# Kernel optimization log

Measured on AMD Instinct MI355X. Metric: run time of the kernel, lower is better.

## Reference

```python
import jax, jax.numpy as jnp
import numpy as np

ANG_RES = 5
USE_MASK = True
EPS = 1e-12  # torch F.normalize eps


def setup_inputs() -> dict:
    key = jax.random.key(0)
    kq, kk, kv = jax.random.split(key, 3)
    shape = (4, 64, 25, 64, 64)  # (b, c, n=angRes^2, h, w)
    return {
        "token_q": jax.random.normal(kq, shape, dtype=jnp.float32),
        "token_k": jax.random.normal(kk, shape, dtype=jnp.float32),
        "token_v": jax.random.normal(kv, shape, dtype=jnp.float32),
    }


def _unfold(x, u):
    # 'b c (u v) h w -> b (h u) (c v w)'
    b, c, n, h, w = x.shape
    v = n // u
    x = x.reshape(b, c, u, v, h, w)
    x = x.transpose(0, 4, 2, 1, 3, 5)  # (b, h, u, c, v, w)
    return x.reshape(b, h * u, c * v * w)


def _fold(x, u, c, h, w):
    # 'b (h u) (c v w) -> b c (u v) h w'
    b = x.shape[0]
    v = u
    x = x.reshape(b, h, u, c, v, w)
    x = x.transpose(0, 3, 2, 4, 1, 5)  # (b, c, u, v, h, w)
    return x.reshape(b, c, u * v, h, w)


def _l2norm(x, axis):
    n = jnp.sqrt(jnp.sum(x * x, axis=axis, keepdims=True))
    return x / jnp.maximum(n, EPS)


def reference(token_q, token_k, token_v):
    b, c, n, h, w = token_q.shape
    u = ANG_RES
    q = _l2norm(_unfold(token_q, u), axis=-1)   # (b, S, D), S=h*u, D=c*u*w
    k = _l2norm(_unfold(token_k, u), axis=-1)   # normalize along feature dim (dim=-2 of k^T)
    vv = _unfold(token_v, u)
    att = jnp.einsum('bsd,btd->bst', q, k)      # cosine similarity scores (b, S, S)
    if USE_MASK:
        S = att.shape[-1]
        causal = jnp.tril(jnp.ones((S, S), dtype=bool))
        att = jnp.where(causal, att, jnp.float32(-1e15))
    att = jax.nn.softmax(att, axis=-1)
    out = jnp.einsum('bst,btd->bsd', att, vv)
    return _fold(out, u, c, h, w) + token_v
```

## Files before the change

### kernel.cpp

```cpp
#include <hip/hip_runtime.h>


#define STR_B 6553600
#define STR_C 102400
#define STR_N 4096
#define STR_H 64

typedef __bf16 bf16x8 __attribute__((ext_vector_type(8)));
typedef float f32x4 __attribute__((ext_vector_type(4)));
typedef unsigned int u32x4 __attribute__((ext_vector_type(4)));

__device__ __forceinline__ int taddr(int b, int s, int d) {
    int h = s / 5, u = s % 5;
    int c = d / 320;
    int r = d % 320;
    int v = r >> 6;
    int w = r & 63;
    return b * STR_B + c * STR_C + (u * 5 + v) * STR_N + h * STR_H + w;
}

__device__ __forceinline__ unsigned short f2bf(float f) {
    unsigned int u = __float_as_uint(f);
    u += 0x7fffu + ((u >> 16) & 1u);
    return (unsigned short)(u >> 16);
}

__device__ __forceinline__ u32x4 pack8(float4 v0, float4 v1) {
    u32x4 w;
    w.x = (unsigned)f2bf(v0.x) | ((unsigned)f2bf(v0.y) << 16);
    w.y = (unsigned)f2bf(v0.z) | ((unsigned)f2bf(v0.w) << 16);
    w.z = (unsigned)f2bf(v1.x) | ((unsigned)f2bf(v1.y) << 16);
    w.w = (unsigned)f2bf(v1.z) | ((unsigned)f2bf(v1.w) << 16);
    return w;
}

__device__ __forceinline__ void gload_lds16(const void* g, void* l) {
    __builtin_amdgcn_global_load_lds(
        (const __attribute__((address_space(1))) unsigned int*)g,
        (__attribute__((address_space(3))) unsigned int*)l,
        16, 0, 0);
}


__global__ __launch_bounds__(1024) void qk_prep_kernel(
        const float* __restrict__ q, const float* __restrict__ k,
        unsigned short* __restrict__ qb, unsigned short* __restrict__ kb,
        float* __restrict__ qinv, float* __restrict__ kinv) {
    int row = blockIdx.x;
    const float* src = (row < 1280) ? q : k;
    unsigned short* dst = (row < 1280) ? qb : kb;
    float* dinv = (row < 1280) ? qinv : kinv;
    int rr = (row < 1280) ? row : row - 1280;
    int b = rr / 320, s = rr % 320;
    int tid = threadIdx.x;
    unsigned short* drow = dst + (size_t)rr * 20480;
    float ss = 0.f;
#pragma unroll
    for (int p = 0; p < 5; ++p) {
        int d = (p * 1024 + tid) * 4;
        f32x4 v = __builtin_nontemporal_load((const f32x4*)(src + taddr(b, s, d)));
        ushort4 w;
        w.x = f2bf(v.x);
        w.y = f2bf(v.y);
        w.z = f2bf(v.z);
        w.w = f2bf(v.w);
        *(ushort4*)(drow + d) = w;
        ss += v.x * v.x + v.y * v.y + v.z * v.z + v.w * v.w;
    }
#pragma unroll
    for (int off = 32; off > 0; off >>= 1) ss += __shfl_xor(ss, off, 64);
    __shared__ float part[16];
    if ((tid & 63) == 0) part[tid >> 6] = ss;
    __syncthreads();
    if (tid == 0) {
        float tot = 0.f;
#pragma unroll
        for (int i = 0; i < 16; ++i) tot += part[i];
        dinv[rr] = 1.f / fmaxf(sqrtf(tot), 1e-12f);
    }
}

#define SPLIT 20
#define KC (20480 / SPLIT)

__global__ __launch_bounds__(256) void scores2_kernel(
        const unsigned short* __restrict__ qb, const unsigned short* __restrict__ kb,
        const float* __restrict__ qinv, const float* __restrict__ kinv,
        float* __restrict__ att) {
    __shared__ unsigned short lds_a[64 * 32];
    __shared__ unsigned short lds_b[64 * 32];
    int b = blockIdx.y;
    int tileid = blockIdx.x / SPLIT;
    int chunk = blockIdx.x % SPLIT;
    int si = 0, rem = tileid;
    while (rem > si) { rem -= (si + 1); ++si; }
    int ti = rem;
    int s0 = si * 64, t0 = ti * 64;

    int tid = threadIdx.x;
    int r = tid >> 2, cl = tid & 3;
    int cg = cl ^ ((r >> 1) & 3);
    const unsigned short* ga = qb + (size_t)(b * 320 + s0 + r) * 20480 + chunk * KC + cg * 8;
    const unsigned short* gk = kb + (size_t)(b * 320 + t0 + r) * 20480 + chunk * KC + cg * 8;
    unsigned short* la = &lds_a[tid * 8];
    unsigned short* lb = &lds_b[tid * 8];

    int lane = tid & 63, wid = tid >> 6;
    int wy = wid >> 1, wx = wid & 1;
    int quad = lane >> 4, l15 = lane & 15;

    f32x4 acc[2][2] = {};
    for (int kk = 0; kk < KC; kk += 32) {
        gload_lds16(ga, la);
        gload_lds16(gk, lb);
        ga += 32; gk += 32;
        __syncthreads();
        bf16x8 af[2], bf[2];
#pragma unroll
        for (int t = 0; t < 2; ++t) {
            int ra = wy * 32 + t * 16 + l15;
            int ca = quad ^ ((ra >> 1) & 3);
            af[t] = __builtin_bit_cast(bf16x8, *(const u32x4*)&lds_a[ra * 32 + ca * 8]);
            int rb = wx * 32 + t * 16 + l15;
            int cb = quad ^ ((rb >> 1) & 3);
            bf[t] = __builtin_bit_cast(bf16x8, *(const u32x4*)&lds_b[rb * 32 + cb * 8]);
        }
        __syncthreads();
#pragma unroll
        for (int tm = 0; tm < 2; ++tm)
#pragma unroll
            for (int tn = 0; tn < 2; ++tn)
                acc[tm][tn] = __builtin_amdgcn_mfma_f32_16x16x32_bf16(
                    af[tm], bf[tn], acc[tm][tn], 0, 0, 0);
    }
    float ki[2];
#pragma unroll
    for (int tn = 0; tn < 2; ++tn)
        ki[tn] = kinv[b * 320 + t0 + wx * 32 + tn * 16 + l15];
#pragma unroll
    for (int tm = 0; tm < 2; ++tm)
#pragma unroll
        for (int tn = 0; tn < 2; ++tn)
#pragma unroll
            for (int i = 0; i < 4; ++i) {
                int s = s0 + wy * 32 + tm * 16 + quad * 4 + i;
                int t = t0 + wx * 32 + tn * 16 + l15;
                if (t <= s)
                    atomicAdd(&att[(b * 320 + s) * 320 + t],
                              acc[tm][tn][i] * qinv[b * 320 + s] * ki[tn]);
            }
}

__global__ __launch_bounds__(256) void softmax_kernel(
        const float* __restrict__ att, unsigned short* __restrict__ p) {
    int row = blockIdx.x * 4 + (threadIdx.x >> 6);
    int lane = threadIdx.x & 63;
    int b = row / 320, s = row % 320;
    const float* ar = att + (b * 320 + s) * 320;
    float v[5];
    float m = -1e30f;
#pragma unroll
    for (int j = 0; j < 5; ++j) {
        int t = lane + j * 64;
        v[j] = (t <= s) ? ar[t] : -1e30f;
        m = fmaxf(m, v[j]);
    }
#pragma unroll
    for (int off = 32; off > 0; off >>= 1) m = fmaxf(m, __shfl_xor(m, off, 64));
    float sum = 0.f;
#pragma unroll
    for (int j = 0; j < 5; ++j) {
        int t = lane + j * 64;
        v[j] = (t <= s) ? __expf(v[j] - m) : 0.f;
        sum += v[j];
    }
#pragma unroll
    for (int off = 32; off > 0; off >>= 1) sum += __shfl_xor(sum, off, 64);
    float inv = 1.f / sum;
    unsigned short* pr = p + (b * 320 + s) * 320;
#pragma unroll
    for (int j = 0; j < 5; ++j) {
        int t = lane + j * 64;
        pr[t] = f2bf(v[j] * inv);
    }
}

__global__ __launch_bounds__(256) void v_prep_kernel(
        const float* __restrict__ vin, unsigned short* __restrict__ vT) {
    __shared__ unsigned short lt[64 * 68];
    int b = blockIdx.z;
    int t0 = blockIdx.y * 64;
    int d0 = blockIdx.x * 64;
    int tid = threadIdx.x;
    int tl0 = tid >> 4;
    int dl = (tid & 15) * 4;
#pragma unroll
    for (int p = 0; p < 4; ++p) {
        int tl = tl0 + p * 16;
        float4 v = *(const float4*)(vin + taddr(b, t0 + tl, d0 + dl));
        lt[(dl + 0) * 68 + tl] = f2bf(v.x);
        lt[(dl + 1) * 68 + tl] = f2bf(v.y);
        lt[(dl + 2) * 68 + tl] = f2bf(v.z);
        lt[(dl + 3) * 68 + tl] = f2bf(v.w);
    }
    __syncthreads();
    int tc = (tid & 15) * 4;
#pragma unroll
    for (int p = 0; p < 4; ++p) {
        int dr = tl0 + p * 16;
        ushort4 w;
        w.x = lt[dr * 68 + tc + 0];
        w.y = lt[dr * 68 + tc + 1];
        w.z = lt[dr * 68 + tc + 2];
        w.w = lt[dr * 68 + tc + 3];
        *(ushort4*)(vT + (size_t)(b * 20480 + d0 + dr) * 320 + t0 + tc) = w;
    }
}

__global__ __launch_bounds__(256) void pv2_kernel(
        const unsigned short* __restrict__ p, const unsigned short* __restrict__ vT,
        const float* __restrict__ vin, float* __restrict__ out) {
    __shared__ unsigned short lds_a[64 * 32];
    __shared__ unsigned short lds_b[64 * 32];
    int b = blockIdx.z;
    int s0 = blockIdx.y * 64;
    int d0 = blockIdx.x * 64;
    int tid = threadIdx.x;
    int r = tid >> 2, cl = tid & 3;
    int cg = cl ^ ((r >> 1) & 3);
    const unsigned short* ga = p + (size_t)(b * 320 + s0 + r) * 320 + cg * 8;
    const unsigned short* gv = vT + (size_t)(b * 20480 + d0 + r) * 320 + cg * 8;
    unsigned short* la = &lds_a[tid * 8];
    unsigned short* lb = &lds_b[tid * 8];

    int lane = tid & 63, wid = tid >> 6;
    int wy = wid >> 1, wx = wid & 1;
    int quad = lane >> 4, l15 = lane & 15;

    f32x4 acc[2][2] = {};
    int nk = (s0 + 64) >> 5;
    for (int kc = 0; kc < nk; ++kc) {
        gload_lds16(ga, la);
        gload_lds16(gv, lb);
        ga += 32; gv += 32;
        __syncthreads();
        bf16x8 af[2], bf[2];
#pragma unroll
        for (int t = 0; t < 2; ++t) {
            int ra = wy * 32 + t * 16 + l15;
            int ca = quad ^ ((ra >> 1) & 3);
            af[t] = __builtin_bit_cast(bf16x8, *(const u32x4*)&lds_a[ra * 32 + ca * 8]);
            int rb = wx * 32 + t * 16 + l15;
            int cb = quad ^ ((rb >> 1) & 3);
            bf[t] = __builtin_bit_cast(bf16x8, *(const u32x4*)&lds_b[rb * 32 + cb * 8]);
        }
        __syncthreads();
#pragma unroll
        for (int tm = 0; tm < 2; ++tm)
#pragma unroll
            for (int tn = 0; tn < 2; ++tn)
                acc[tm][tn] = __builtin_amdgcn_mfma_f32_16x16x32_bf16(
                    af[tm], bf[tn], acc[tm][tn], 0, 0, 0);
    }
#pragma unroll
    for (int tm = 0; tm < 2; ++tm)
#pragma unroll
        for (int tn = 0; tn < 2; ++tn)
#pragma unroll
            for (int i = 0; i < 4; ++i) {
                int s = s0 + wy * 32 + tm * 16 + quad * 4 + i;
                int d = d0 + wx * 32 + tn * 16 + l15;
                int a = taddr(b, s, d);
                out[a] = acc[tm][tn][i] + vin[a];
            }
}


__global__ __launch_bounds__(256) void norm_kernel(
        const float* __restrict__ q, const float* __restrict__ k,
        float* __restrict__ qinv, float* __restrict__ kinv) {
    int row = blockIdx.x;
    const float* src = (row < 1280) ? q : k;
    float* dst = (row < 1280) ? qinv : kinv;
    int rr = (row < 1280) ? row : row - 1280;
    int b = rr / 320, s = rr % 320;
    int tid = threadIdx.x;
    float ss = 0.f;
#pragma unroll
    for (int p = 0; p < 20; ++p) {
        int kk = (p * 256 + tid) * 4;
        const float4 v = *(const float4*)(src + taddr(b, s, kk));
        ss += v.x * v.x + v.y * v.y + v.z * v.z + v.w * v.w;
    }
#pragma unroll
    for (int off = 32; off > 0; off >>= 1) ss += __shfl_xor(ss, off, 64);
    __shared__ float part[4];
    if ((tid & 63) == 0) part[tid >> 6] = ss;
    __syncthreads();
    if (tid == 0) {
        float tot = part[0] + part[1] + part[2] + part[3];
        dst[rr] = 1.f / fmaxf(sqrtf(tot), 1e-12f);
    }
}

#define CHUNKS 10
#define KCHUNK 2048

__global__ __launch_bounds__(256) void scores_kernel(
        const float* __restrict__ q, const float* __restrict__ kmat,
        const float* __restrict__ qinv, const float* __restrict__ kinv,
        float* __restrict__ att) {
    __shared__ unsigned short lds_a[64 * 40];
    __shared__ unsigned short lds_b[64 * 40];
    int b = blockIdx.y;
    int tileid = blockIdx.x / CHUNKS;
    int chunk = blockIdx.x % CHUNKS;
    int si = 0, rem = tileid;
    while (rem > si) { rem -= (si + 1); ++si; }
    int ti = rem;
    int s0 = si * 64, t0 = ti * 64;
    int tid = threadIdx.x;
    int r = tid >> 2, koff = (tid & 3) * 8;
    int lane = tid & 63, wid = tid >> 6;
    int wy = wid >> 1, wx = wid & 1;
    int quad = lane >> 4, l15 = lane & 15;
    f32x4 acc[2][2] = {};
    for (int kk = 0; kk < KCHUNK; kk += 32) {
        int kg = chunk * KCHUNK + kk + koff;
        const float4* pa = (const float4*)(q + taddr(b, s0 + r, kg));
        *(u32x4*)&lds_a[r * 40 + koff] = pack8(pa[0], pa[1]);
        const float4* pb = (const float4*)(kmat + taddr(b, t0 + r, kg));
        *(u32x4*)&lds_b[r * 40 + koff] = pack8(pb[0], pb[1]);
        __syncthreads();
        bf16x8 af[2], bf[2];
#pragma unroll
        for (int t = 0; t < 2; ++t) {
            af[t] = __builtin_bit_cast(bf16x8,
                *(const u32x4*)&lds_a[(wy * 32 + t * 16 + l15) * 40 + quad * 8]);
            bf[t] = __builtin_bit_cast(bf16x8,
                *(const u32x4*)&lds_b[(wx * 32 + t * 16 + l15) * 40 + quad * 8]);
        }
#pragma unroll
        for (int tm = 0; tm < 2; ++tm)
#pragma unroll
            for (int tn = 0; tn < 2; ++tn)
                acc[tm][tn] = __builtin_amdgcn_mfma_f32_16x16x32_bf16(
                    af[tm], bf[tn], acc[tm][tn], 0, 0, 0);
        __syncthreads();
    }
#pragma unroll
    for (int tm = 0; tm < 2; ++tm)
#pragma unroll
        for (int tn = 0; tn < 2; ++tn)
#pragma unroll
            for (int i = 0; i < 4; ++i) {
                int s = s0 + wy * 32 + tm * 16 + quad * 4 + i;
                int t = t0 + wx * 32 + tn * 16 + l15;
                if (t <= s) {
                    float val = acc[tm][tn][i] * qinv[b * 320 + s] * kinv[b * 320 + t];
                    atomicAdd(&att[(b * 320 + s) * 320 + t], val);
                }
            }
}

__global__ __launch_bounds__(256) void pv_kernel(
        const unsigned short* __restrict__ p, const float* __restrict__ vin,
        float* __restrict__ out) {
    __shared__ unsigned short lds_a[64 * 40];
    __shared__ unsigned short lds_b[64 * 40];
    int b = blockIdx.z;
    int s0 = blockIdx.y * 64;
    int d0 = blockIdx.x * 64;
    int tid = threadIdx.x;
    int lane = tid & 63, wid = tid >> 6;
    int wy = wid >> 1, wx = wid & 1;
    int quad = lane >> 4, l15 = lane & 15;
    int ar = tid >> 2, akoff = (tid & 3) * 8;
    int bt = tid >> 4;
    int bd = (tid & 15) * 4;
    f32x4 acc[2][2] = {};
    int nk = (s0 + 64) >> 5;
    for (int kc = 0; kc < nk; ++kc) {
        int t0k = kc * 32;
        u32x4 aw = *(const u32x4*)(p + ((b * 320 + s0 + ar) * 320 + t0k + akoff));
        *(u32x4*)&lds_a[ar * 40 + akoff] = aw;
#pragma unroll
        for (int pp = 0; pp < 2; ++pp) {
            int tt = bt + pp * 16;
            float4 v = *(const float4*)(vin + taddr(b, t0k + tt, d0 + bd));
            lds_b[(bd + 0) * 40 + tt] = f2bf(v.x);
            lds_b[(bd + 1) * 40 + tt] = f2bf(v.y);
            lds_b[(bd + 2) * 40 + tt] = f2bf(v.z);
            lds_b[(bd + 3) * 40 + tt] = f2bf(v.w);
        }
        __syncthreads();
        bf16x8 af[2], bf[2];
#pragma unroll
        for (int t = 0; t < 2; ++t) {
            af[t] = __builtin_bit_cast(bf16x8,
                *(const u32x4*)&lds_a[(wy * 32 + t * 16 + l15) * 40 + quad * 8]);
            bf[t] = __builtin_bit_cast(bf16x8,
                *(const u32x4*)&lds_b[(wx * 32 + t * 16 + l15) * 40 + quad * 8]);
        }
#pragma unroll
        for (int tm = 0; tm < 2; ++tm)
#pragma unroll
            for (int tn = 0; tn < 2; ++tn)
                acc[tm][tn] = __builtin_amdgcn_mfma_f32_16x16x32_bf16(
                    af[tm], bf[tn], acc[tm][tn], 0, 0, 0);
        __syncthreads();
    }
#pragma unroll
    for (int tm = 0; tm < 2; ++tm)
#pragma unroll
        for (int tn = 0; tn < 2; ++tn)
#pragma unroll
            for (int i = 0; i < 4; ++i) {
                int s = s0 + wy * 32 + tm * 16 + quad * 4 + i;
                int d = d0 + wx * 32 + tn * 16 + l15;
                int a = taddr(b, s, d);
                out[a] = acc[tm][tn][i] + vin[a];
            }
}

extern "C" void kernel_launch(void* const* d_in, const int* in_sizes, int n_in,
                              void* d_out, int out_size, void* d_ws, size_t ws_size,
                              hipStream_t stream) {
    const float* q = (const float*)d_in[0];
    const float* k = (const float*)d_in[1];
    const float* v = (const float*)d_in[2];
    float* out = (float*)d_out;
    char* ws = (char*)d_ws;

    const size_t QB_BYTES = (size_t)4 * 320 * 20480 * 2;
    const size_t ATT_BYTES = (size_t)4 * 320 * 320 * 4;
    const size_t P_BYTES = (size_t)4 * 320 * 320 * 2;
    const size_t INV_BYTES = (size_t)4 * 320 * 4;
    const size_t NEED = 2 * QB_BYTES + ATT_BYTES + P_BYTES + 2 * INV_BYTES;

    if (ws_size >= NEED) {
        unsigned short* qb = (unsigned short*)ws;
        unsigned short* kb = (unsigned short*)(ws + QB_BYTES);
        float* att = (float*)(ws + 2 * QB_BYTES);
        unsigned short* p = (unsigned short*)(ws + 2 * QB_BYTES + ATT_BYTES);
        float* qinv = (float*)(ws + 2 * QB_BYTES + ATT_BYTES + P_BYTES);
        float* kinv = (float*)(ws + 2 * QB_BYTES + ATT_BYTES + P_BYTES + INV_BYTES);
        unsigned short* vT = (unsigned short*)ws;

        qk_prep_kernel<<<2560, 1024, 0, stream>>>(q, k, qb, kb, qinv, kinv);
        hipMemsetAsync(att, 0, ATT_BYTES, stream);
        scores2_kernel<<<dim3(15 * SPLIT, 4), 256, 0, stream>>>(qb, kb, qinv, kinv, att);
        softmax_kernel<<<320, 256, 0, stream>>>(att, p);
        v_prep_kernel<<<dim3(320, 5, 4), 256, 0, stream>>>(v, vT);
        pv2_kernel<<<dim3(320, 5, 4), 256, 0, stream>>>(p, vT, v, out);
    } else {
        float* qinv = (float*)ws;
        float* kinv = (float*)(ws + 5120);
        float* att = (float*)(ws + 10240);
        unsigned short* p = (unsigned short*)(ws + 10240 + ATT_BYTES);

        norm_kernel<<<2560, 256, 0, stream>>>(q, k, qinv, kinv);
        hipMemsetAsync(att, 0, ATT_BYTES, stream);
        scores_kernel<<<dim3(15 * CHUNKS, 4), 256, 0, stream>>>(q, k, qinv, kinv, att);
        softmax_kernel<<<320, 256, 0, stream>>>(att, p);
        pv_kernel<<<dim3(320, 5, 4), 256, 0, stream>>>(p, v, out);
    }
}
```

Before: 420.9 us.

## Double-buffer LDS in QK and PV GEMMs; fuse softmax with V transpose

The scores and PV kernels now use two LDS buffers per operand, issuing the global-to-LDS load for the next k-step before computing on the current one, so each k-step needs one barrier instead of two. The softmax and V-transpose kernels are merged into one launch whose first 320 blocks do softmax and the rest transpose V. This targets load latency exposed in the GEMM loops and one kernel launch gap. In exchange it doubles LDS per block, which may reduce occupancy. The merged kernel also makes softmax blocks reserve the transpose scratch LDS.

```diff
diff --git a/kernel.cpp b/kernel.cpp
--- a/kernel.cpp
+++ b/kernel.cpp
@@ -40,6 +40,26 @@
         (__attribute__((address_space(3))) unsigned int*)l,
         16, 0, 0);
 }
+
+#define QK_STEP(LA, LB)                                                          \
+    do {                                                                         \
+        bf16x8 af[2], bf[2];                                                     \
+        _Pragma("unroll")                                                        \
+        for (int t = 0; t < 2; ++t) {                                            \
+            int ra = wy * 32 + t * 16 + l15;                                     \
+            int ca = quad ^ ((ra >> 1) & 3);                                     \
+            af[t] = __builtin_bit_cast(bf16x8, *(const u32x4*)&LA[ra * 32 + ca * 8]); \
+            int rb = wx * 32 + t * 16 + l15;                                     \
+            int cb = quad ^ ((rb >> 1) & 3);                                     \
+            bf[t] = __builtin_bit_cast(bf16x8, *(const u32x4*)&LB[rb * 32 + cb * 8]); \
+        }                                                                        \
+        _Pragma("unroll")                                                        \
+        for (int tm = 0; tm < 2; ++tm)                                           \
+            _Pragma("unroll")                                                    \
+            for (int tn = 0; tn < 2; ++tn)                                       \
+                acc[tm][tn] = __builtin_amdgcn_mfma_f32_16x16x32_bf16(           \
+                    af[tm], bf[tn], acc[tm][tn], 0, 0, 0);                       \
+    } while (0)
 
 
 __global__ __launch_bounds__(1024) void qk_prep_kernel(
@@ -87,8 +107,10 @@
         const unsigned short* __restrict__ qb, const unsigned short* __restrict__ kb,
         const float* __restrict__ qinv, const float* __restrict__ kinv,
         float* __restrict__ att) {
-    __shared__ unsigned short lds_a[64 * 32];
-    __shared__ unsigned short lds_b[64 * 32];
+    __shared__ unsigned short lds_a0[64 * 32];
+    __shared__ unsigned short lds_a1[64 * 32];
+    __shared__ unsigned short lds_b0[64 * 32];
+    __shared__ unsigned short lds_b1[64 * 32];
     int b = blockIdx.y;
     int tileid = blockIdx.x / SPLIT;
     int chunk = blockIdx.x % SPLIT;
@@ -100,38 +122,32 @@
     int tid = threadIdx.x;
     int r = tid >> 2, cl = tid & 3;
     int cg = cl ^ ((r >> 1) & 3);
-    const unsigned short* ga = qb + (size_t)(b * 320 + s0 + r) * 20480 + chunk * KC + cg * 8;
-    const unsigned short* gk = kb + (size_t)(b * 320 + t0 + r) * 20480 + chunk * KC + cg * 8;
-    unsigned short* la = &lds_a[tid * 8];
-    unsigned short* lb = &lds_b[tid * 8];
+    const unsigned short* gab = qb + (size_t)(b * 320 + s0 + r) * 20480 + chunk * KC + cg * 8;
+    const unsigned short* gkb = kb + (size_t)(b * 320 + t0 + r) * 20480 + chunk * KC + cg * 8;
+    unsigned short* la0 = &lds_a0[tid * 8];
+    unsigned short* la1 = &lds_a1[tid * 8];
+    unsigned short* lb0 = &lds_b0[tid * 8];
+    unsigned short* lb1 = &lds_b1[tid * 8];
 
     int lane = tid & 63, wid = tid >> 6;
     int wy = wid >> 1, wx = wid & 1;
     int quad = lane >> 4, l15 = lane & 15;
 
     f32x4 acc[2][2] = {};
-    for (int kk = 0; kk < KC; kk += 32) {
-        gload_lds16(ga, la);
-        gload_lds16(gk, lb);
-        ga += 32; gk += 32;
-        __syncthreads();
-        bf16x8 af[2], bf[2];
-#pragma unroll
-        for (int t = 0; t < 2; ++t) {
-            int ra = wy * 32 + t * 16 + l15;
-            int ca = quad ^ ((ra >> 1) & 3);
-            af[t] = __builtin_bit_cast(bf16x8, *(const u32x4*)&lds_a[ra * 32 + ca * 8]);
-            int rb = wx * 32 + t * 16 + l15;
-            int cb = quad ^ ((rb >> 1) & 3);
-            bf[t] = __builtin_bit_cast(bf16x8, *(const u32x4*)&lds_b[rb * 32 + cb * 8]);
-        }
-        __syncthreads();
-#pragma unroll
-        for (int tm = 0; tm < 2; ++tm)
-#pragma unroll
-            for (int tn = 0; tn < 2; ++tn)
-                acc[tm][tn] = __builtin_amdgcn_mfma_f32_16x16x32_bf16(
-                    af[tm], bf[tn], acc[tm][tn], 0, 0, 0);
+    gload_lds16(gab, la0);
+    gload_lds16(gkb, lb0);
+    __syncthreads();
+    for (int kk = 0; kk < KC; kk += 64) {
+        gload_lds16(gab + kk + 32, la1);
+        gload_lds16(gkb + kk + 32, lb1);
+        QK_STEP(lds_a0, lds_b0);
+        __syncthreads();
+        if (kk + 64 < KC) {
+            gload_lds16(gab + kk + 64, la0);
+            gload_lds16(gkb + kk + 64, lb0);
+        }
+        QK_STEP(lds_a1, lds_b1);
+        __syncthreads();
     }
     float ki[2];
 #pragma unroll
@@ -149,6 +165,156 @@
                     atomicAdd(&att[(b * 320 + s) * 320 + t],
                               acc[tm][tn][i] * qinv[b * 320 + s] * ki[tn]);
             }
+}
+
+__global__ __launch_bounds__(256) void softmax_vprep_kernel(
+        const float* __restrict__ att, unsigned short* __restrict__ p,
+        const float* __restrict__ vin, unsigned short* __restrict__ vT) {
+    __shared__ unsigned short lt[64 * 68];
+    int bid = blockIdx.x;
+    int tid = threadIdx.x;
+    if (bid < 320) {
+        int row = bid * 4 + (tid >> 6);
+        int lane = tid & 63;
+        int b = row / 320, s = row % 320;
+        const float* ar = att + (b * 320 + s) * 320;
+        float v[5];
+        float m = -1e30f;
+#pragma unroll
+        for (int j = 0; j < 5; ++j) {
+            int t = lane + j * 64;
+            v[j] = (t <= s) ? ar[t] : -1e30f;
+            m = fmaxf(m, v[j]);
+        }
+#pragma unroll
+        for (int off = 32; off > 0; off >>= 1) m = fmaxf(m, __shfl_xor(m, off, 64));
+        float sum = 0.f;
+#pragma unroll
+        for (int j = 0; j < 5; ++j) {
+            int t = lane + j * 64;
+            v[j] = (t <= s) ? __expf(v[j] - m) : 0.f;
+            sum += v[j];
+        }
+#pragma unroll
+        for (int off = 32; off > 0; off >>= 1) sum += __shfl_xor(sum, off, 64);
+        float inv = 1.f / sum;
+        unsigned short* pr = p + (b * 320 + s) * 320;
+#pragma unroll
+        for (int j = 0; j < 5; ++j) {
+            int t = lane + j * 64;
+            pr[t] = f2bf(v[j] * inv);
+        }
+        return;
+    }
+    int idx = bid - 320;
+    int d0 = (idx % 320) * 64;
+    int t0 = ((idx / 320) % 5) * 64;
+    int b = idx / 1600;
+    int tl0 = tid >> 4;
+    int dl = (tid & 15) * 4;
+#pragma unroll
+    for (int pp = 0; pp < 4; ++pp) {
+        int tl = tl0 + pp * 16;
+        float4 v = *(const float4*)(vin + taddr(b, t0 + tl, d0 + dl));
+        lt[(dl + 0) * 68 + tl] = f2bf(v.x);
+        lt[(dl + 1) * 68 + tl] = f2bf(v.y);
+        lt[(dl + 2) * 68 + tl] = f2bf(v.z);
+        lt[(dl + 3) * 68 + tl] = f2bf(v.w);
+    }
+    __syncthreads();
+    int tc = (tid & 15) * 4;
+#pragma unroll
+    for (int pp = 0; pp < 4; ++pp) {
+        int dr = tl0 + pp * 16;
+        ushort4 w;
+        w.x = lt[dr * 68 + tc + 0];
+        w.y = lt[dr * 68 + tc + 1];
+        w.z = lt[dr * 68 + tc + 2];
+        w.w = lt[dr * 68 + tc + 3];
+        *(ushort4*)(vT + (size_t)(b * 20480 + d0 + dr) * 320 + t0 + tc) = w;
+    }
+}
+
+__global__ __launch_bounds__(256) void pv2_kernel(
+        const unsigned short* __restrict__ p, const unsigned short* __restrict__ vT,
+        const float* __restrict__ vin, float* __restrict__ out) {
+    __shared__ unsigned short lds_a0[64 * 32];
+    __shared__ unsigned short lds_a1[64 * 32];
+    __shared__ unsigned short lds_b0[64 * 32];
+    __shared__ unsigned short lds_b1[64 * 32];
+    int b = blockIdx.z;
+    int s0 = blockIdx.y * 64;
+    int d0 = blockIdx.x * 64;
+    int tid = threadIdx.x;
+    int r = tid >> 2, cl = tid & 3;
+    int cg = cl ^ ((r >> 1) & 3);
+    const unsigned short* gab = p + (size_t)(b * 320 + s0 + r) * 320 + cg * 8;
+    const unsigned short* gvb = vT + (size_t)(b * 20480 + d0 + r) * 320 + cg * 8;
+    unsigned short* la0 = &lds_a0[tid * 8];
+    unsigned short* la1 = &lds_a1[tid * 8];
+    unsigned short* lb0 = &lds_b0[tid * 8];
+    unsigned short* lb1 = &lds_b1[tid * 8];
+
+    int lane = tid & 63, wid = tid >> 6;
+    int wy = wid >> 1, wx = wid & 1;
+    int quad = lane >> 4, l15 = lane & 15;
+
+    f32x4 acc[2][2] = {};
+    int nk = (s0 + 64) >> 5;
+    gload_lds16(gab, la0);
+    gload_lds16(gvb, lb0);
+    __syncthreads();
+    for (int kc = 0; kc < nk; kc += 2) {
+        gload_lds16(gab + (kc + 1) * 32, la1);
+        gload_lds16(gvb + (kc + 1) * 32, lb1);
+        QK_STEP(lds_a0, lds_b0);
+        __syncthreads();
+        if (kc + 2 < nk) {
+            gload_lds16(gab + (kc + 2) * 32, la0);
+            gload_lds16(gvb + (kc + 2) * 32, lb0);
+        }
+        QK_STEP(lds_a1, lds_b1);
+        __syncthreads();
+    }
+#pragma unroll
+    for (int tm = 0; tm < 2; ++tm)
+#pragma unroll
+        for (int tn = 0; tn < 2; ++tn)
+#pragma unroll
+            for (int i = 0; i < 4; ++i) {
+                int s = s0 + wy * 32 + tm * 16 + quad * 4 + i;
+                int d = d0 + wx * 32 + tn * 16 + l15;
+                int a = taddr(b, s, d);
+                out[a] = acc[tm][tn][i] + vin[a];
+            }
+}
+
+
+__global__ __launch_bounds__(256) void norm_kernel(
+        const float* __restrict__ q, const float* __restrict__ k,
+        float* __restrict__ qinv, float* __restrict__ kinv) {
+    int row = blockIdx.x;
+    const float* src = (row < 1280) ? q : k;
+    float* dst = (row < 1280) ? qinv : kinv;
+    int rr = (row < 1280) ? row : row - 1280;
+    int b = rr / 320, s = rr % 320;
+    int tid = threadIdx.x;
+    float ss = 0.f;
+#pragma unroll
+    for (int p = 0; p < 20; ++p) {
+        int kk = (p * 256 + tid) * 4;
+        const float4 v = *(const float4*)(src + taddr(b, s, kk));
+        ss += v.x * v.x + v.y * v.y + v.z * v.z + v.w * v.w;
+    }
+#pragma unroll
+    for (int off = 32; off > 0; off >>= 1) ss += __shfl_xor(ss, off, 64);
+    __shared__ float part[4];
+    if ((tid & 63) == 0) part[tid >> 6] = ss;
+    __syncthreads();
+    if (tid == 0) {
+        float tot = part[0] + part[1] + part[2] + part[3];
+        dst[rr] = 1.f / fmaxf(sqrtf(tot), 1e-12f);
+    }
 }
 
 __global__ __launch_bounds__(256) void softmax_kernel(
@@ -182,124 +348,6 @@
     for (int j = 0; j < 5; ++j) {
         int t = lane + j * 64;
         pr[t] = f2bf(v[j] * inv);
-    }
-}
-
-__global__ __launch_bounds__(256) void v_prep_kernel(
-        const float* __restrict__ vin, unsigned short* __restrict__ vT) {
-    __shared__ unsigned short lt[64 * 68];
-    int b = blockIdx.z;
-    int t0 = blockIdx.y * 64;
-    int d0 = blockIdx.x * 64;
-    int tid = threadIdx.x;
-    int tl0 = tid >> 4;
-    int dl = (tid & 15) * 4;
-#pragma unroll
-    for (int p = 0; p < 4; ++p) {
-        int tl = tl0 + p * 16;
-        float4 v = *(const float4*)(vin + taddr(b, t0 + tl, d0 + dl));
-        lt[(dl + 0) * 68 + tl] = f2bf(v.x);
-        lt[(dl + 1) * 68 + tl] = f2bf(v.y);
-        lt[(dl + 2) * 68 + tl] = f2bf(v.z);
-        lt[(dl + 3) * 68 + tl] = f2bf(v.w);
-    }
-    __syncthreads();
-    int tc = (tid & 15) * 4;
-#pragma unroll
-    for (int p = 0; p < 4; ++p) {
-        int dr = tl0 + p * 16;
-        ushort4 w;
-        w.x = lt[dr * 68 + tc + 0];
-        w.y = lt[dr * 68 + tc + 1];
-        w.z = lt[dr * 68 + tc + 2];
-        w.w = lt[dr * 68 + tc + 3];
-        *(ushort4*)(vT + (size_t)(b * 20480 + d0 + dr) * 320 + t0 + tc) = w;
-    }
-}
-
-__global__ __launch_bounds__(256) void pv2_kernel(
-        const unsigned short* __restrict__ p, const unsigned short* __restrict__ vT,
-        const float* __restrict__ vin, float* __restrict__ out) {
-    __shared__ unsigned short lds_a[64 * 32];
-    __shared__ unsigned short lds_b[64 * 32];
-    int b = blockIdx.z;
-    int s0 = blockIdx.y * 64;
-    int d0 = blockIdx.x * 64;
-    int tid = threadIdx.x;
-    int r = tid >> 2, cl = tid & 3;
-    int cg = cl ^ ((r >> 1) & 3);
-    const unsigned short* ga = p + (size_t)(b * 320 + s0 + r) * 320 + cg * 8;
-    const unsigned short* gv = vT + (size_t)(b * 20480 + d0 + r) * 320 + cg * 8;
-    unsigned short* la = &lds_a[tid * 8];
-    unsigned short* lb = &lds_b[tid * 8];
-
-    int lane = tid & 63, wid = tid >> 6;
-    int wy = wid >> 1, wx = wid & 1;
-    int quad = lane >> 4, l15 = lane & 15;
-
-    f32x4 acc[2][2] = {};
-    int nk = (s0 + 64) >> 5;
-    for (int kc = 0; kc < nk; ++kc) {
-        gload_lds16(ga, la);
-        gload_lds16(gv, lb);
-        ga += 32; gv += 32;
-        __syncthreads();
-        bf16x8 af[2], bf[2];
-#pragma unroll
-        for (int t = 0; t < 2; ++t) {
-            int ra = wy * 32 + t * 16 + l15;
-            int ca = quad ^ ((ra >> 1) & 3);
-            af[t] = __builtin_bit_cast(bf16x8, *(const u32x4*)&lds_a[ra * 32 + ca * 8]);
-            int rb = wx * 32 + t * 16 + l15;
-            int cb = quad ^ ((rb >> 1) & 3);
-            bf[t] = __builtin_bit_cast(bf16x8, *(const u32x4*)&lds_b[rb * 32 + cb * 8]);
-        }
-        __syncthreads();
-#pragma unroll
-        for (int tm = 0; tm < 2; ++tm)
-#pragma unroll
-            for (int tn = 0; tn < 2; ++tn)
-                acc[tm][tn] = __builtin_amdgcn_mfma_f32_16x16x32_bf16(
-                    af[tm], bf[tn], acc[tm][tn], 0, 0, 0);
-    }
-#pragma unroll
-    for (int tm = 0; tm < 2; ++tm)
-#pragma unroll
-        for (int tn = 0; tn < 2; ++tn)
-#pragma unroll
-            for (int i = 0; i < 4; ++i) {
-                int s = s0 + wy * 32 + tm * 16 + quad * 4 + i;
-                int d = d0 + wx * 32 + tn * 16 + l15;
-                int a = taddr(b, s, d);
-                out[a] = acc[tm][tn][i] + vin[a];
-            }
-}
-
-
-__global__ __launch_bounds__(256) void norm_kernel(
-        const float* __restrict__ q, const float* __restrict__ k,
-        float* __restrict__ qinv, float* __restrict__ kinv) {
-    int row = blockIdx.x;
-    const float* src = (row < 1280) ? q : k;
-    float* dst = (row < 1280) ? qinv : kinv;
-    int rr = (row < 1280) ? row : row - 1280;
-    int b = rr / 320, s = rr % 320;
-    int tid = threadIdx.x;
-    float ss = 0.f;
-#pragma unroll
-    for (int p = 0; p < 20; ++p) {
-        int kk = (p * 256 + tid) * 4;
-        const float4 v = *(const float4*)(src + taddr(b, s, kk));
-        ss += v.x * v.x + v.y * v.y + v.z * v.z + v.w * v.w;
-    }
-#pragma unroll
-    for (int off = 32; off > 0; off >>= 1) ss += __shfl_xor(ss, off, 64);
-    __shared__ float part[4];
-    if ((tid & 63) == 0) part[tid >> 6] = ss;
-    __syncthreads();
-    if (tid == 0) {
-        float tot = part[0] + part[1] + part[2] + part[3];
-        dst[rr] = 1.f / fmaxf(sqrtf(tot), 1e-12f);
     }
 }
 
@@ -450,8 +498,7 @@
         qk_prep_kernel<<<2560, 1024, 0, stream>>>(q, k, qb, kb, qinv, kinv);
         hipMemsetAsync(att, 0, ATT_BYTES, stream);
         scores2_kernel<<<dim3(15 * SPLIT, 4), 256, 0, stream>>>(qb, kb, qinv, kinv, att);
-        softmax_kernel<<<320, 256, 0, stream>>>(att, p);
-        v_prep_kernel<<<dim3(320, 5, 4), 256, 0, stream>>>(v, vT);
+        softmax_vprep_kernel<<<6720, 256, 0, stream>>>(att, p, v, vT);
         pv2_kernel<<<dim3(320, 5, 4), 256, 0, stream>>>(p, vT, v, out);
     } else {
         float* qinv = (float*)ws;
```

New measurement: 414.2 us. Within noise of the previous version (-1.6%).
